# Performance work log

Measured on AMD Instinct MI355X. Metric: run time of the kernel, lower is better.

The kernel has to match this reference:

```python
import jax, jax.numpy as jnp
import numpy as np

N_NODES = 30000
N_REL = 200
N_EDGES = 150000
N_EDGES_NHOP = 30000
NFEAT = 100
NHID = 100
REL_DIM = 100
NHEADS = 2
ALPHA = 0.2  # leaky relu slope


def setup_inputs() -> dict:
    key = jax.random.key(0)
    ks = jax.random.split(key, 16)
    s = 0.1
    D = NHEADS * NHID
    inp = {}
    inp["entity_embeddings"] = jax.random.normal(ks[0], (N_NODES, NFEAT), jnp.float32)
    inp["relation_embed"] = jax.random.normal(ks[1], (N_REL, REL_DIM), jnp.float32)
    inp["edge_list"] = jax.random.randint(ks[2], (2, N_EDGES), 0, N_NODES)
    inp["edge_type"] = jax.random.randint(ks[3], (N_EDGES,), 0, N_REL)
    inp["edge_embed"] = jax.random.normal(ks[4], (N_EDGES, REL_DIM), jnp.float32)
    inp["edge_list_nhop"] = jax.random.randint(ks[5], (2, N_EDGES_NHOP), 0, N_NODES)
    inp["edge_type_nhop"] = jax.random.randint(ks[6], (N_EDGES_NHOP, 2), 0, N_REL)
    inp["entity_embeddings_mapping"] = jax.random.normal(ks[7], (N_NODES, NFEAT), jnp.float32)
    # learned params (xavier-like scale)
    inp["a_heads"] = jax.random.normal(ks[8], (NHEADS, NHID, 2 * NFEAT + REL_DIM), jnp.float32) * s
    inp["a2_heads"] = jax.random.normal(ks[9], (NHEADS, NHID), jnp.float32) * s
    inp["W"] = jax.random.normal(ks[10], (REL_DIM, D), jnp.float32) * s
    inp["a_out"] = jax.random.normal(ks[11], (D, 3 * D), jnp.float32) * s
    inp["a2_out"] = jax.random.normal(ks[12], (D,), jnp.float32) * s
    return inp


def _att_layer(x, src, dst, edge_embed, a, a2, n_nodes, concat):
    # Sparse graph attention (KBGAT style). a: [out, 2*in + rel_dim].
    in_dim = x.shape[1]
    a_src, a_dst, a_rel = a[:, :in_dim], a[:, in_dim:2 * in_dim], a[:, 2 * in_dim:]
    # edge_m = a @ cat(x[src], x[dst], edge_embed)^T, computed without the big concat
    edge_m = x[src] @ a_src.T + x[dst] @ a_dst.T + edge_embed @ a_rel.T  # [E, out]
    powers = -jax.nn.leaky_relu(edge_m @ a2, ALPHA)                      # [E]
    edge_e = jnp.exp(powers)                                             # [E]
    e_rowsum = jax.ops.segment_sum(edge_e, src, num_segments=n_nodes)    # [N]
    e_rowsum = jnp.where(e_rowsum == 0.0, 1e-12, e_rowsum)
    h = jax.ops.segment_sum(edge_e[:, None] * edge_m, src, num_segments=n_nodes)  # [N, out]
    h = h / e_rowsum[:, None]
    return jax.nn.elu(h) if concat else h


def reference(entity_embeddings, relation_embed, edge_list, edge_type, edge_embed,
              edge_list_nhop, edge_type_nhop, entity_embeddings_mapping,
              a_heads, a2_heads, W, a_out, a2_out):
    N = entity_embeddings.shape[0]
    src = jnp.concatenate([edge_list[0], edge_list_nhop[0]])
    dst = jnp.concatenate([edge_list[1], edge_list_nhop[1]])
    # 2-hop edge embedding = sum of the two relation embeddings on the path
    ee_nhop = relation_embed[edge_type_nhop[:, 0]] + relation_embed[edge_type_nhop[:, 1]]
    ee1 = jnp.concatenate([edge_embed, ee_nhop], axis=0)
    h1 = _att_layer(entity_embeddings, src, dst, ee1, a_heads[0], a2_heads[0], N, True)
    h2 = _att_layer(entity_embeddings, src, dst, ee1, a_heads[1], a2_heads[1], N, True)
    h = jnp.concatenate([h1, h2], axis=1)  # [N, 2*nhid]; dropout p=0 (eval)
    out_relation = relation_embed @ W      # [R, 2*nhid]
    ee2 = jnp.concatenate([out_relation[edge_type],
                           out_relation[edge_type_nhop[:, 0]] + out_relation[edge_type_nhop[:, 1]]],
                          axis=0)
    out_entity = _att_layer(h, src, dst, ee2, a_out, a2_out, N, False)
    return jax.nn.elu(out_entity), out_relation
```

## Files before the change

kernel.cpp:

```cpp
#include <hip/hip_runtime.h>

#define N_NODES 30000
#define E1 150000
#define EN 30000
#define ET 180000
#define LALPHA 0.2f
#define NB_SCAN 118

typedef unsigned int u32;
typedef unsigned short u16;
typedef __attribute__((ext_vector_type(8))) short short8;
typedef __attribute__((ext_vector_type(4))) short short4v;
typedef __attribute__((ext_vector_type(4))) float f32x4;

__device__ __forceinline__ float bf2f(u16 u){ return __uint_as_float(((u32)u)<<16); }
__device__ __forceinline__ float2 bfp2(u32 u){
  return make_float2(__uint_as_float(u<<16), __uint_as_float(u & 0xffff0000u));
}
__device__ __forceinline__ u16 f2bf(float f){
  u32 x = __float_as_uint(f);
  return (u16)((x + 0x7fffu + ((x>>16)&1u)) >> 16);
}
__device__ __forceinline__ u32 pk(float x, float y){
  return ((u32)f2bf(x)) | (((u32)f2bf(y))<<16);
}
__device__ __forceinline__ float wredf(float v){
  #pragma unroll
  for(int o=32;o>0;o>>=1) v += __shfl_xor(v, o, 64);
  return v;
}
__device__ __forceinline__ float eluf(float y){ return (y>0.f)? y : expm1f(y); }
__device__ __forceinline__ float ld1(const void* p, int i, int f){
  return f ? ((const float*)p)[i] : bf2f(((const u16*)p)[i]);
}
__device__ __forceinline__ float2 ldp(const void* p, int i, int f){
  if(f){ return ((const float2*)p)[i]; }
  return bfp2(((const u32*)p)[i]);
}
__device__ __forceinline__ void st1(void* p, int i, float v, int f){
  if(f) ((float*)p)[i] = v; else ((u16*)p)[i] = f2bf(v);
}

__device__ __forceinline__ short8 frag_zero(){
  short8 r;
  #pragma unroll
  for(int i=0;i<8;i++) r[i]=0;
  return r;
}
__device__ __forceinline__ short8 ldfragb(const u16* p, int idx){
  short8 r;
  short4v lo = *(const short4v*)(p+idx);
  short4v hi = *(const short4v*)(p+idx+4);
  #pragma unroll
  for(int i=0;i<4;i++){ r[i]=lo[i]; r[4+i]=hi[i]; }
  return r;
}
__device__ __forceinline__ short8 ldfragb_p4(const u16* p, int idx){
  short8 r=frag_zero();
  short4v lo = *(const short4v*)(p+idx);
  #pragma unroll
  for(int i=0;i<4;i++) r[i]=lo[i];
  return r;
}
__device__ __forceinline__ short8 ldfrag(const void* p, int idx, int f){
  short8 r;
  if(f){
    const float* fp=(const float*)p+idx;
    #pragma unroll
    for(int i=0;i<8;i++) r[i]=(short)f2bf(fp[i]);
  } else {
    return ldfragb((const u16*)p, idx);
  }
  return r;
}
__device__ __forceinline__ short8 ldfrag_p4(const void* p, int idx, int f){
  short8 r=frag_zero();
  if(f){
    const float* fp=(const float*)p+idx;
    #pragma unroll
    for(int i=0;i<4;i++) r[i]=(short)f2bf(fp[i]);
  } else {
    return ldfragb_p4((const u16*)p, idx);
  }
  return r;
}

__global__ void k_detect(const u32* x, int* flag){
  int t = threadIdx.x;
  int c = 0;
  #pragma unroll
  for(int i=0;i<4;i++){
    u32 v = x[t*4+i];
    u32 lo = v & 0xffffu;
    u32 e = (lo>>7)&0xffu;
    c += (lo==0u || (e>=100u && e<=140u)) ? 1 : 0;
  }
  __shared__ int sd[256];
  sd[t]=c; __syncthreads();
  for(int o=128;o>0;o>>=1){ if(t<o) sd[t]+=sd[t+o]; __syncthreads(); }
  if(t==0) *flag = (sd[0] > 512) ? 0 : 1;
}

__global__ void k_prep(const void* ent, const void* ah, const void* ao, const void* ee,
                       u16* entB, u16* ahB, u16* aoB, u16* eeB, int ws_ok, const int* flag){
  int f = *flag;
  int gid = blockIdx.x*256 + threadIdx.x;
  int stride = gridDim.x*256;
  const int T0=750000, T1=765000, T2=795000, T3=795000+3750000;
  int lim = (f && ws_ok) ? T3 : T2;
  for(int i=gid; i<lim; i+=stride){
    const void* src; u16* dst; int g;
    if(i<T0){ src=ent; dst=entB; g=i; }
    else if(i<T1){ src=ah; dst=ahB; g=i-T0; }
    else if(i<T2){ src=ao; dst=aoB; g=i-T1; }
    else { src=ee; dst=eeB; g=i-T2; }
    if(f){
      float4 v = ((const float4*)src)[g];
      short4v o;
      o[0]=(short)f2bf(v.x); o[1]=(short)f2bf(v.y);
      o[2]=(short)f2bf(v.z); o[3]=(short)f2bf(v.w);
      ((short4v*)dst)[g] = o;
    } else {
      ((short4v*)dst)[g] = ((const short4v*)src)[g];
    }
  }
}

__global__ void k_outrel(const void* rel, const void* W, float* outrel, void* out, const int* flag){
  int f = *flag;
  int t = blockIdx.x*blockDim.x + threadIdx.x;
  if(t >= 200*200) return;
  int r = t / 200, j = t - r*200;
  float acc = 0.f;
  for(int k=0;k<100;k++) acc += ld1(rel, r*100+k, f) * ld1(W, k*200+j, f);
  outrel[t] = acc;
  st1(out, 6000000 + t, acc, f);
}

__global__ void k_small_b(const void* ah, const void* a2h, const void* ao, const void* a2o,
                          float* b1, float* b2, const int* flag){
  int f = *flag;
  int i = blockIdx.x*4 + (threadIdx.x>>6);
  int L = threadIdx.x & 63;
  if(i >= 1200) return;
  float a = 0.f;
  if(i < 600){
    int hd = i/300, k = i - hd*300;
    for(int j=L; j<100; j+=64)
      a += ld1(a2h, hd*100+j, f) * ld1(ah, hd*30000 + j*300 + k, f);
    a = wredf(a);
    if(L==0) b1[i] = a;
  } else {
    int k = i - 600;
    for(int j=L; j<200; j+=64)
      a += ld1(a2o, j, f) * ld1(ao, j*600 + k, f);
    a = wredf(a);
    if(L==0) b2[k] = a;
  }
}

__global__ void k_small_c(const void* rel, const float* outrel, const float* b1, const float* b2,
                          float* c1, float* c2, const int* flag){
  int f = *flag;
  int i = blockIdx.x*4 + (threadIdx.x>>6);
  int L = threadIdx.x & 63;
  if(i >= 600) return;
  float a = 0.f;
  if(i < 400){
    int hd = i/200, r = i - hd*200;
    for(int k=L; k<100; k+=64)
      a += b1[hd*300+200+k] * ld1(rel, r*100+k, f);
    a = wredf(a);
    if(L==0) c1[i] = a;
  } else {
    int r = i - 400;
    for(int k=L; k<200; k+=64)
      a += b2[400+k] * outrel[r*200+k];
    a = wredf(a);
    if(L==0) c2[r] = a;
  }
}

__global__ void k_count(const int* src1, const int* srcN, int* cnt){
  int e = blockIdx.x*256 + threadIdx.x;
  if(e>=ET) return;
  int s = (e<E1)? src1[e] : srcN[e-E1];
  atomicAdd(&cnt[s],1);
}

__global__ void k_scan1(const int* cnt, int* ofs, int* bsum){
  __shared__ int sd[256];
  int b=blockIdx.x, t=threadIdx.x;
  int idx=b*256+t;
  int v=(idx<N_NODES)? cnt[idx] : 0;
  sd[t]=v; __syncthreads();
  for(int o=1;o<256;o<<=1){
    int u=(t>=o)? sd[t-o]:0;
    __syncthreads();
    sd[t]+=u; __syncthreads();
  }
  if(idx<N_NODES) ofs[idx]=sd[t]-v;
  if(t==255) bsum[b]=sd[255];
}

__global__ void k_scan2(const int* bsum, int* bstart, int* ofs){
  __shared__ int sd[128];
  int t=threadIdx.x;
  int v=(t<NB_SCAN)? bsum[t]:0;
  sd[t]=v; __syncthreads();
  for(int o=1;o<128;o<<=1){
    int u=(t>=o)? sd[t-o]:0;
    __syncthreads();
    sd[t]+=u; __syncthreads();
  }
  if(t<NB_SCAN) bstart[t]=sd[t]-v;
  if(t==127) ofs[N_NODES]=sd[127];
}

__global__ void k_scan3(int* ofs, int* cur, const int* bstart){
  int b=blockIdx.x, t=threadIdx.x;
  int idx=b*256+t;
  if(idx>=N_NODES) return;
  int v = ofs[idx] + bstart[b];
  ofs[idx]=v; cur[idx]=v;
}

__global__ void k_scatter(const int* src1, const int* srcN, int* cur, int* eord){
  int e = blockIdx.x*256 + threadIdx.x;
  if(e>=ET) return;
  int s = (e<E1)? src1[e] : srcN[e-E1];
  int p = atomicAdd(&cur[s],1);
  eord[p]=e;
}

__global__ void k_q1(const u32* entB2, const float* b1, float* q1){
  int n = blockIdx.x*4 + (threadIdx.x>>6);
  if(n>=N_NODES) return;
  int L = threadIdx.x & 63;
  float d00=0,d01=0,d10=0,d11=0;
  if(L<50){
    float2 xv = bfp2(entB2[n*50+L]);
    int k0=2*L;
    d00 = xv.x*b1[k0]     + xv.y*b1[k0+1];
    d01 = xv.x*b1[100+k0] + xv.y*b1[100+k0+1];
    d10 = xv.x*b1[300+k0] + xv.y*b1[300+k0+1];
    d11 = xv.x*b1[400+k0] + xv.y*b1[400+k0+1];
  }
  d00=wredf(d00); d01=wredf(d01); d10=wredf(d10); d11=wredf(d11);
  if(L==0){ q1[n*4+0]=d00; q1[n*4+1]=d01; q1[n*4+2]=d10; q1[n*4+3]=d11; }
}

__global__ __launch_bounds__(256) void k_edge1g(const void* ee, const u16* eeB, int ws_ok,
    const int* src1, const int* dst1, const float* b1, const float* q1,
    float* w1, const int* flag){
  int f = *flag;
  const void* eeP = (f && ws_ok) ? (const void*)eeB : ee;
  int fe = (f && ws_ok) ? 0 : f;
  int wid = threadIdx.x>>6, l = threadIdx.x&63;
  int lr = l&15, lg = l>>4;
  int m0 = blockIdx.x*128 + wid*32;
  short8 bfr[4];
  #pragma unroll
  for(int ks=0;ks<4;ks++){
    int kb = ks*32 + lg*8;
    short8 b = frag_zero();
    if(lr<2){
      const float* bp = b1 + (lr==0? 200:500);
      #pragma unroll
      for(int i=0;i<8;i++){ int k=kb+i; if(k<100) b[i]=(short)f2bf(bp[k]); }
    }
    bfr[ks]=b;
  }
  int row0 = m0 + lr, row1 = m0 + 16 + lr;
  bool ok0 = row0 < E1, ok1 = row1 < E1;
  f32x4 acc0=(f32x4){0,0,0,0}, acc1=(f32x4){0,0,0,0};
  #pragma unroll
  for(int ks=0;ks<4;ks++){
    int kb = ks*32 + lg*8;
    short8 a0 = frag_zero(), a1 = frag_zero();
    if(ok0){
      if(kb+8<=100) a0 = ldfrag(eeP, row0*100+kb, fe);
      else if(kb<100) a0 = ldfrag_p4(eeP, row0*100+kb, fe);
    }
    if(ok1){
      if(kb+8<=100) a1 = ldfrag(eeP, row1*100+kb, fe);
      else if(kb<100) a1 = ldfrag_p4(eeP, row1*100+kb, fe);
    }
    acc0 = __builtin_amdgcn_mfma_f32_16x16x32_bf16(a0, bfr[ks], acc0, 0,0,0);
    acc1 = __builtin_amdgcn_mfma_f32_16x16x32_bf16(a1, bfr[ks], acc1, 0,0,0);
  }
  if(lr<2){
    #pragma unroll
    for(int mi=0;mi<2;mi++){
      #pragma unroll
      for(int r=0;r<4;r++){
        int e = m0 + mi*16 + lg*4 + r;
        if(e<E1){
          float rv = (mi==0)? acc0[r] : acc1[r];
          int s=src1[e], d=dst1[e];
          float p = q1[s*4+lr*2] + q1[d*4+lr*2+1] + rv;
          p = (p>=0.f)? p : LALPHA*p;
          w1[2*e + lr] = expf(-p);
        }
      }
    }
  }
}

__global__ void k_edge1b(const int* etn, const int* srcN, const int* dstN,
                         const float* c1, const float* q1, float* w1){
  int en = blockIdx.x*256+threadIdx.x;
  if(en>=EN) return;
  int t0=etn[en*2], t1=etn[en*2+1];
  float r0 = c1[t0]+c1[t1];
  float r1 = c1[200+t0]+c1[200+t1];
  int s=srcN[en], d=dstN[en];
  float p0 = q1[s*4+0]+q1[d*4+1]+r0;
  float p1 = q1[s*4+2]+q1[d*4+3]+r1;
  p0=(p0>=0.f)?p0:LALPHA*p0;
  p1=(p1>=0.f)?p1:LALPHA*p1;
  w1[2*(E1+en)]   = expf(-p0);
  w1[2*(E1+en)+1] = expf(-p1);
}

__global__ void k_acc1(const int* ofs, const int* eord,
                       const int* dst1, const int* dstN, const int* etn,
                       const u32* entB2, const void* ee, const u32* eeB32, int ws_ok,
                       const void* rel,
                       const float2* w1p, u32* Gq, float* rs1, const int* flag){
  int f = *flag;
  int use_pack = (f==1) && ws_ok;
  int n = blockIdx.x*4 + (threadIdx.x>>6);
  if(n>=N_NODES) return;
  int L = threadIdx.x & 63;
  int beg = ofs[n], end = ofs[n+1];
  float av0x=0,av0y=0,av1x=0,av1y=0, aw0x=0,aw0y=0,aw1x=0,aw1y=0;
  float r0=0, r1=0;
  int i = beg;
  for(; i+3<end; i+=4){
    int e[4]; float2 w[4]; int d[4];
    #pragma unroll
    for(int u=0;u<4;u++) e[u]=eord[i+u];
    #pragma unroll
    for(int u=0;u<4;u++){ w[u]=w1p[e[u]]; d[u]=(e[u]<E1)? dst1[e[u]] : dstN[e[u]-E1]; }
    r0 += w[0].x+w[1].x+w[2].x+w[3].x;
    r1 += w[0].y+w[1].y+w[2].y+w[3].y;
    if(L<50){
      float2 xv[4], vv[4];
      #pragma unroll
      for(int u=0;u<4;u++) xv[u]=bfp2(entB2[d[u]*50+L]);
      #pragma unroll
      for(int u=0;u<4;u++){
        if(e[u]<E1){ vv[u] = use_pack? bfp2(eeB32[e[u]*50+L]) : ldp(ee, e[u]*50+L, f); }
        else { int en=e[u]-E1; int t0=etn[en*2], t1=etn[en*2+1];
               float2 a=ldp(rel,t0*50+L,f), b=ldp(rel,t1*50+L,f);
               vv[u]=make_float2(a.x+b.x, a.y+b.y); }
      }
      #pragma unroll
      for(int u=0;u<4;u++){
        av0x += w[u].x*xv[u].x; av0y += w[u].x*xv[u].y;
        av1x += w[u].y*xv[u].x; av1y += w[u].y*xv[u].y;
        aw0x += w[u].x*vv[u].x; aw0y += w[u].x*vv[u].y;
        aw1x += w[u].y*vv[u].x; aw1y += w[u].y*vv[u].y;
      }
    }
  }
  for(; i<end; ++i){
    int e0 = eord[i];
    float2 wa = w1p[e0];
    r0 += wa.x; r1 += wa.y;
    int d0 = (e0<E1)? dst1[e0] : dstN[e0-E1];
    if(L<50){
      float2 x0 = bfp2(entB2[d0*50+L]);
      float2 v0;
      if(e0<E1){ v0 = use_pack? bfp2(eeB32[e0*50+L]) : ldp(ee, e0*50+L, f); }
      else { int en=e0-E1; int t0=etn[en*2], t1=etn[en*2+1];
             float2 a=ldp(rel,t0*50+L,f), b=ldp(rel,t1*50+L,f);
             v0=make_float2(a.x+b.x, a.y+b.y); }
      av0x += wa.x*x0.x; av0y += wa.x*x0.y;
      av1x += wa.y*x0.x; av1y += wa.y*x0.y;
      aw0x += wa.x*v0.x; aw0y += wa.x*v0.y;
      aw1x += wa.y*v0.x; aw1y += wa.y*v0.y;
    }
  }
  float i0 = (r0==0.f)? 0.f : 1.f/r0;
  float i1 = (r1==0.f)? 0.f : 1.f/r1;
  if(L<50){
    u32* g0 = Gq + n*100;
    u32* g1 = Gq + 3000000 + n*100;
    g0[L]    = pk(av0x*i0, av0y*i0);
    g0[50+L] = pk(aw0x*i0, aw0y*i0);
    g1[L]    = pk(av1x*i1, av1y*i1);
    g1[50+L] = pk(aw1x*i1, aw1y*i1);
  }
  if(L==0){ rs1[n]=r0; rs1[N_NODES+n]=r1; }
}

__global__ __launch_bounds__(256) void k_gemm1m(const u16* G, const u16* ahB, const u16* entB,
                        const float* rs1, u16* h){
  int hd = blockIdx.y;
  int wid = threadIdx.x>>6, l = threadIdx.x&63;
  int lr = l&15, lg = l>>4;
  int m0 = blockIdx.x*32;
  int row0 = m0 + lr, row1 = m0 + 16 + lr;
  bool hi_ok = (m0+16) < N_NODES;
  const u16* Gh0 = G + hd*6000000 + row0*200;
  const u16* Gh1 = G + hd*6000000 + row1*200;
  const u16* A = ahB + hd*30000;
  f32x4 acc[2][2];
  #pragma unroll
  for(int mi=0;mi<2;mi++)
    #pragma unroll
    for(int ntl=0;ntl<2;ntl++) acc[mi][ntl]=(f32x4){0.f,0.f,0.f,0.f};
  #pragma unroll
  for(int k0=0;k0<100;k0+=32){
    int kb = k0 + lg*8;
    short8 a0 = (kb+8<=100)? ldfragb(entB, row0*100+kb)
              : (kb<100    ? ldfragb_p4(entB, row0*100+kb) : frag_zero());
    short8 a1 = frag_zero();
    if(hi_ok){
      if(kb+8<=100) a1 = ldfragb(entB, row1*100+kb);
      else if(kb<100) a1 = ldfragb_p4(entB, row1*100+kb);
    }
    #pragma unroll
    for(int ntl=0;ntl<2;ntl++){
      int j = (ntl*4+wid)*16 + lr;
      short8 b = frag_zero();
      if(j<100){
        if(kb+8<=100) b = ldfragb(A, j*300 + kb);
        else if(kb<100) b = ldfragb_p4(A, j*300 + kb);
      }
      acc[0][ntl] = __builtin_amdgcn_mfma_f32_16x16x32_bf16(a0, b, acc[0][ntl], 0,0,0);
      acc[1][ntl] = __builtin_amdgcn_mfma_f32_16x16x32_bf16(a1, b, acc[1][ntl], 0,0,0);
    }
  }
  #pragma unroll
  for(int k0=0;k0<200;k0+=32){
    int kb = k0 + lg*8;
    short8 a0 = (kb+8<=200)? ldfragb(Gh0, kb) : frag_zero();
    short8 a1 = (hi_ok && kb+8<=200)? ldfragb(Gh1, kb) : frag_zero();
    #pragma unroll
    for(int ntl=0;ntl<2;ntl++){
      int j = (ntl*4+wid)*16 + lr;
      short8 b = (j<100 && kb+8<=200)? ldfragb(A, j*300 + 100 + kb) : frag_zero();
      acc[0][ntl] = __builtin_amdgcn_mfma_f32_16x16x32_bf16(a0, b, acc[0][ntl], 0,0,0);
      acc[1][ntl] = __builtin_amdgcn_mfma_f32_16x16x32_bf16(a1, b, acc[1][ntl], 0,0,0);
    }
  }
  #pragma unroll
  for(int mi=0;mi<2;mi++){
    if(mi==1 && !hi_ok) break;
    #pragma unroll
    for(int r=0;r<4;r++){
      int rr = m0 + mi*16 + lg*4 + r;
      float sc = (rs1[hd*N_NODES+rr]==0.f)? 0.f : 1.f;
      #pragma unroll
      for(int ntl=0;ntl<2;ntl++){
        int j = (ntl*4+wid)*16 + lr;
        if(j<100) h[rr*200 + hd*100 + j] = f2bf(eluf(acc[mi][ntl][r]*sc));
      }
    }
  }
}

__global__ void k_q2(const u32* h32, const float* b2, float* q2){
  int n = blockIdx.x*4 + (threadIdx.x>>6);
  if(n>=N_NODES) return;
  int L = threadIdx.x&63;
  float ds=0, dd=0;
  if(L<50){
    float2 a = bfp2(h32[n*100+2*L]);
    float2 b = bfp2(h32[n*100+2*L+1]);
    int k0=4*L;
    ds = a.x*b2[k0]+a.y*b2[k0+1]+b.x*b2[k0+2]+b.y*b2[k0+3];
    dd = a.x*b2[200+k0]+a.y*b2[200+k0+1]+b.x*b2[200+k0+2]+b.y*b2[200+k0+3];
  }
  ds=wredf(ds); dd=wredf(dd);
  if(L==0){ q2[n*2]=ds; q2[n*2+1]=dd; }
}

__global__ void k_edge2(const int* src1,const int* dst1,const int* srcN,const int* dstN,
                        const int* et, const int* etn, const float* c2, const float* q2, float* w2){
  int e = blockIdx.x*256+threadIdx.x;
  if(e>=ET) return;
  int s,d; float r;
  if(e<E1){ s=src1[e]; d=dst1[e]; r = c2[et[e]]; }
  else { int en=e-E1; s=srcN[en]; d=dstN[en]; r = c2[etn[en*2]]+c2[etn[en*2+1]]; }
  float p = q2[s*2] + q2[d*2+1] + r;
  p = (p>=0.f)? p : LALPHA*p;
  w2[e] = expf(-p);
}

__global__ void k_acc2(const int* ofs, const int* eord,
                       const int* dst1,const int* dstN, const int* et,const int* etn,
                       const u32* h32, const float4* or4, const float* w2,
                       u32* Gq, float* rs2){
  const uint2* h2 = (const uint2*)h32;
  int n = blockIdx.x*4 + (threadIdx.x>>6);
  if(n>=N_NODES) return;
  int L = threadIdx.x&63;
  int beg=ofs[n], end=ofs[n+1];
  float rv=0;
  float avx=0,avy=0,avz=0,avw=0, awx=0,awy=0,awz=0,aww=0;
  int i=beg;
  for(; i+3<end; i+=4){
    int e[4]; float wv[4]; int d[4];
    #pragma unroll
    for(int u=0;u<4;u++) e[u]=eord[i+u];
    #pragma unroll
    for(int u=0;u<4;u++){ wv[u]=w2[e[u]]; d[u]=(e[u]<E1)? dst1[e[u]]:dstN[e[u]-E1]; }
    rv += wv[0]+wv[1]+wv[2]+wv[3];
    if(L<50){
      float2 ha[4], hb[4]; float4 o[4];
      #pragma unroll
      for(int u=0;u<4;u++){ uint2 hv = h2[d[u]*50+L]; ha[u]=bfp2(hv.x); hb[u]=bfp2(hv.y); }
      #pragma unroll
      for(int u=0;u<4;u++){
        if(e[u]<E1){ o[u] = or4[et[e[u]]*50+L]; }
        else { int en=e[u]-E1; float4 a=or4[etn[en*2]*50+L], b=or4[etn[en*2+1]*50+L];
               o[u]=make_float4(a.x+b.x,a.y+b.y,a.z+b.z,a.w+b.w); }
      }
      #pragma unroll
      for(int u=0;u<4;u++){
        avx += wv[u]*ha[u].x; avy += wv[u]*ha[u].y;
        avz += wv[u]*hb[u].x; avw += wv[u]*hb[u].y;
        awx += wv[u]*o[u].x;  awy += wv[u]*o[u].y;
        awz += wv[u]*o[u].z;  aww += wv[u]*o[u].w;
      }
    }
  }
  for(; i<end; ++i){
    int e0=eord[i];
    float w0=w2[e0];
    rv += w0;
    int d0 = (e0<E1)? dst1[e0]:dstN[e0-E1];
    if(L<50){
      uint2 hv = h2[d0*50+L];
      float2 ha0=bfp2(hv.x), hb0=bfp2(hv.y);
      float4 o0;
      if(e0<E1){ o0 = or4[et[e0]*50+L]; }
      else { int en=e0-E1; float4 a=or4[etn[en*2]*50+L], b=or4[etn[en*2+1]*50+L];
             o0=make_float4(a.x+b.x,a.y+b.y,a.z+b.z,a.w+b.w); }
      avx += w0*ha0.x; avy += w0*ha0.y; avz += w0*hb0.x; avw += w0*hb0.y;
      awx += w0*o0.x; awy += w0*o0.y; awz += w0*o0.z; aww += w0*o0.w;
    }
  }
  float inv = (rv==0.f)? 0.f : 1.f/rv;
  if(L<50){
    u32* g = Gq + n*200;
    g[2*L]       = pk(avx*inv, avy*inv);
    g[2*L+1]     = pk(avz*inv, avw*inv);
    g[100+2*L]   = pk(awx*inv, awy*inv);
    g[100+2*L+1] = pk(awz*inv, aww*inv);
  }
  if(L==0) rs2[n]=rv;
}

__global__ __launch_bounds__(256) void k_gemm2m(const u16* G, const u16* aoB, const u16* h,
                        const float* rs2, void* out, const int* flag){
  int f = *flag;
  int wid = threadIdx.x>>6, l = threadIdx.x&63;
  int lr = l&15, lg = l>>4;
  int m0 = blockIdx.x*32;
  int row0 = m0 + lr, row1 = m0 + 16 + lr;
  bool hi_ok = (m0+16) < N_NODES;
  const u16* h0 = h + row0*200;
  const u16* h1 = h + row1*200;
  const u16* g0 = G + row0*400;
  const u16* g1 = G + row1*400;
  f32x4 acc[2][4];
  #pragma unroll
  for(int mi=0;mi<2;mi++)
    #pragma unroll
    for(int ntl=0;ntl<4;ntl++) acc[mi][ntl]=(f32x4){0.f,0.f,0.f,0.f};
  #pragma unroll
  for(int k0=0;k0<200;k0+=32){
    int kb = k0 + lg*8;
    short8 a0 = (kb+8<=200)? ldfragb(h0, kb) : frag_zero();
    short8 a1 = (hi_ok && kb+8<=200)? ldfragb(h1, kb) : frag_zero();
    #pragma unroll
    for(int ntl=0;ntl<4;ntl++){
      int j = (ntl*4+wid)*16 + lr;
      short8 b = (j<200 && kb+8<=200)? ldfragb(aoB, j*600 + kb) : frag_zero();
      acc[0][ntl] = __builtin_amdgcn_mfma_f32_16x16x32_bf16(a0, b, acc[0][ntl], 0,0,0);
      acc[1][ntl] = __builtin_amdgcn_mfma_f32_16x16x32_bf16(a1, b, acc[1][ntl], 0,0,0);
    }
  }
  #pragma unroll
  for(int k0=0;k0<400;k0+=32){
    int kb = k0 + lg*8;
    short8 a0 = (kb+8<=400)? ldfragb(g0, kb) : frag_zero();
    short8 a1 = (hi_ok && kb+8<=400)? ldfragb(g1, kb) : frag_zero();
    #pragma unroll
    for(int ntl=0;ntl<4;ntl++){
      int j = (ntl*4+wid)*16 + lr;
      short8 b = (j<200 && kb+8<=400)? ldfragb(aoB, j*600 + 200 + kb) : frag_zero();
      acc[0][ntl] = __builtin_amdgcn_mfma_f32_16x16x32_bf16(a0, b, acc[0][ntl], 0,0,0);
      acc[1][ntl] = __builtin_amdgcn_mfma_f32_16x16x32_bf16(a1, b, acc[1][ntl], 0,0,0);
    }
  }
  #pragma unroll
  for(int mi=0;mi<2;mi++){
    if(mi==1 && !hi_ok) break;
    #pragma unroll
    for(int r=0;r<4;r++){
      int rr = m0 + mi*16 + lg*4 + r;
      float sc = (rs2[rr]==0.f)? 0.f : 1.f;
      #pragma unroll
      for(int ntl=0;ntl<4;ntl++){
        int j = (ntl*4+wid)*16 + lr;
        if(j<200) st1(out, rr*200 + j, eluf(acc[mi][ntl][r]*sc), f);
      }
    }
  }
}

extern "C" void kernel_launch(void* const* d_in, const int* in_sizes, int n_in,
                              void* d_out, int out_size, void* d_ws, size_t ws_size,
                              hipStream_t stream) {
  const void* ent = d_in[0];
  const void* rel = d_in[1];
  const int* el  = (const int*)d_in[2];
  const int* et  = (const int*)d_in[3];
  const void* ee  = d_in[4];
  const int* eln = (const int*)d_in[5];
  const int* etn = (const int*)d_in[6];
  const void* ah  = d_in[8];
  const void* a2h = d_in[9];
  const void* W   = d_in[10];
  const void* ao  = d_in[11];
  const void* a2o = d_in[12];

  float* wsf    = (float*)d_ws;
  int*   flag   = (int*)wsf;
  float* outrel = wsf+4;
  float* b1     = wsf+40008;
  float* b2     = wsf+40608;
  float* c1     = wsf+41208;
  float* c2     = wsf+41608;
  float* q1     = wsf+41808;
  float* q2     = wsf+161808;
  float* w1     = wsf+221808;
  float* w2     = wsf+581808;
  float* rs1    = wsf+761808;
  float* rs2    = wsf+821808;
  int*   ofs    = (int*)(wsf+851808);
  int*   cnt    = ofs+30001;
  int*   cur    = cnt+30000;
  int*   eord   = cur+30000;
  int*   bsum   = (int*)(wsf+1121812);
  int*   bstart = bsum+128;
  u16*   G      = (u16*)(wsf+1122072);
  u16*   h      = (u16*)(wsf+7122072);
  u16*   entB   = (u16*)(wsf+10122072);
  u16*   ahB    = (u16*)(wsf+11622072);
  u16*   aoB    = (u16*)(wsf+11652072);
  u16*   eeB    = (u16*)(wsf+11712072);
  int ws_ok = (ws_size >= (size_t)19212072*4) ? 1 : 0;

  const int* src1 = el;
  const int* dst1 = el + E1;
  const int* srcN = eln;
  const int* dstN = eln + EN;

  k_detect<<<1,256,0,stream>>>((const u32*)ent, flag);
  hipMemsetAsync(cnt, 0, 30000*sizeof(int), stream);
  k_prep<<<2048,256,0,stream>>>(ent, ah, ao, ee, entB, ahB, aoB, eeB, ws_ok, flag);
  k_small_b<<<300,256,0,stream>>>(ah,a2h,ao,a2o,b1,b2,flag);
  k_outrel<<<(200*200+255)/256,256,0,stream>>>(rel, W, outrel, d_out, flag);
  k_small_c<<<150,256,0,stream>>>(rel, outrel, b1, b2, c1, c2, flag);
  k_count<<<(ET+255)/256,256,0,stream>>>(src1, srcN, cnt);
  k_scan1<<<NB_SCAN,256,0,stream>>>(cnt, ofs, bsum);
  k_scan2<<<1,128,0,stream>>>(bsum, bstart, ofs);
  k_scan3<<<NB_SCAN,256,0,stream>>>(ofs, cur, bstart);
  k_scatter<<<(ET+255)/256,256,0,stream>>>(src1, srcN, cur, eord);
  k_q1<<<(N_NODES+3)/4,256,0,stream>>>((const u32*)entB, b1, q1);
  k_edge1g<<<(E1+127)/128,256,0,stream>>>(ee, eeB, ws_ok, src1, dst1, b1, q1, w1, flag);
  k_edge1b<<<(EN+255)/256,256,0,stream>>>(etn, srcN, dstN, c1, q1, w1);
  k_acc1<<<(N_NODES+3)/4,256,0,stream>>>(ofs, eord, dst1, dstN, etn,
                                         (const u32*)entB, ee, (const u32*)eeB, ws_ok,
                                         rel, (const float2*)w1, (u32*)G, rs1, flag);
  dim3 g1grid((N_NODES+31)/32, 2);
  k_gemm1m<<<g1grid,256,0,stream>>>(G, ahB, entB, rs1, h);
  k_q2<<<(N_NODES+3)/4,256,0,stream>>>((const u32*)h, b2, q2);
  k_edge2<<<(ET+255)/256,256,0,stream>>>(src1, dst1, srcN, dstN, et, etn, c2, q2, w2);
  k_acc2<<<(N_NODES+3)/4,256,0,stream>>>(ofs, eord, dst1, dstN, et, etn,
                                         (const u32*)h, (const float4*)outrel, w2, (u32*)G, rs2);
  k_gemm2m<<<(N_NODES+31)/32,256,0,stream>>>(G, aoB, h, rs2, d_out, flag);
}
```

Baseline: 257.4 us.

## Interleave h and aggregated features into one row buffer for the second GEMM

```diff
diff --git a/kernel.cpp b/kernel.cpp
--- a/kernel.cpp
+++ b/kernel.cpp
@@ -54,6 +54,9 @@
   #pragma unroll
   for(int i=0;i<4;i++){ r[i]=lo[i]; r[4+i]=hi[i]; }
   return r;
+}
+__device__ __forceinline__ short8 ldfragb16(const u16* p, int idx){
+  return *(const short8*)(p+idx);
 }
 __device__ __forceinline__ short8 ldfragb_p4(const u16* p, int idx){
   short8 r=frag_zero();
@@ -397,7 +400,7 @@
 }
 
 __global__ __launch_bounds__(256) void k_gemm1m(const u16* G, const u16* ahB, const u16* entB,
-                        const float* rs1, u16* h){
+                        const float* rs1, u16* Gx2){
   int hd = blockIdx.y;
   int wid = threadIdx.x>>6, l = threadIdx.x&63;
   int lr = l&15, lg = l>>4;
@@ -457,20 +460,21 @@
       #pragma unroll
       for(int ntl=0;ntl<2;ntl++){
         int j = (ntl*4+wid)*16 + lr;
-        if(j<100) h[rr*200 + hd*100 + j] = f2bf(eluf(acc[mi][ntl][r]*sc));
-      }
-    }
-  }
-}
-
-__global__ void k_q2(const u32* h32, const float* b2, float* q2){
+        if(j<100) Gx2[rr*600 + hd*100 + j] = f2bf(eluf(acc[mi][ntl][r]*sc));
+      }
+    }
+  }
+}
+
+__global__ void k_q2(const uint2* hq, const float* b2, float* q2){
   int n = blockIdx.x*4 + (threadIdx.x>>6);
   if(n>=N_NODES) return;
   int L = threadIdx.x&63;
   float ds=0, dd=0;
   if(L<50){
-    float2 a = bfp2(h32[n*100+2*L]);
-    float2 b = bfp2(h32[n*100+2*L+1]);
+    uint2 hv = hq[n*150+L];
+    float2 a = bfp2(hv.x);
+    float2 b = bfp2(hv.y);
     int k0=4*L;
     ds = a.x*b2[k0]+a.y*b2[k0+1]+b.x*b2[k0+2]+b.y*b2[k0+3];
     dd = a.x*b2[200+k0]+a.y*b2[200+k0+1]+b.x*b2[200+k0+2]+b.y*b2[200+k0+3];
@@ -493,9 +497,9 @@
 
 __global__ void k_acc2(const int* ofs, const int* eord,
                        const int* dst1,const int* dstN, const int* et,const int* etn,
-                       const u32* h32, const float4* or4, const float* w2,
-                       u32* Gq, float* rs2){
-  const uint2* h2 = (const uint2*)h32;
+                       u32* Gx2u, const float4* or4, const float* w2,
+                       float* rs2){
+  const uint2* h2 = (const uint2*)Gx2u;
   int n = blockIdx.x*4 + (threadIdx.x>>6);
   if(n>=N_NODES) return;
   int L = threadIdx.x&63;
@@ -513,7 +517,7 @@
     if(L<50){
       float2 ha[4], hb[4]; float4 o[4];
       #pragma unroll
-      for(int u=0;u<4;u++){ uint2 hv = h2[d[u]*50+L]; ha[u]=bfp2(hv.x); hb[u]=bfp2(hv.y); }
+      for(int u=0;u<4;u++){ uint2 hv = h2[d[u]*150+L]; ha[u]=bfp2(hv.x); hb[u]=bfp2(hv.y); }
       #pragma unroll
       for(int u=0;u<4;u++){
         if(e[u]<E1){ o[u] = or4[et[e[u]]*50+L]; }
@@ -535,7 +539,7 @@
     rv += w0;
     int d0 = (e0<E1)? dst1[e0]:dstN[e0-E1];
     if(L<50){
-      uint2 hv = h2[d0*50+L];
+      uint2 hv = h2[d0*150+L];
       float2 ha0=bfp2(hv.x), hb0=bfp2(hv.y);
       float4 o0;
       if(e0<E1){ o0 = or4[et[e0]*50+L]; }
@@ -547,7 +551,7 @@
   }
   float inv = (rv==0.f)? 0.f : 1.f/rv;
   if(L<50){
-    u32* g = Gq + n*200;
+    u32* g = Gx2u + n*300 + 100;
     g[2*L]       = pk(avx*inv, avy*inv);
     g[2*L+1]     = pk(avz*inv, avw*inv);
     g[100+2*L]   = pk(awx*inv, awy*inv);
@@ -556,7 +560,7 @@
   if(L==0) rs2[n]=rv;
 }
 
-__global__ __launch_bounds__(256) void k_gemm2m(const u16* G, const u16* aoB, const u16* h,
+__global__ __launch_bounds__(256) void k_gemm2m(const u16* Gx2, const u16* aoB,
                         const float* rs2, void* out, const int* flag){
   int f = *flag;
   int wid = threadIdx.x>>6, l = threadIdx.x&63;
@@ -564,37 +568,23 @@
   int m0 = blockIdx.x*32;
   int row0 = m0 + lr, row1 = m0 + 16 + lr;
   bool hi_ok = (m0+16) < N_NODES;
-  const u16* h0 = h + row0*200;
-  const u16* h1 = h + row1*200;
-  const u16* g0 = G + row0*400;
-  const u16* g1 = G + row1*400;
+  const u16* a0p = Gx2 + row0*600;
+  const u16* a1p = Gx2 + row1*600;
   f32x4 acc[2][4];
   #pragma unroll
   for(int mi=0;mi<2;mi++)
     #pragma unroll
     for(int ntl=0;ntl<4;ntl++) acc[mi][ntl]=(f32x4){0.f,0.f,0.f,0.f};
   #pragma unroll
-  for(int k0=0;k0<200;k0+=32){
+  for(int k0=0;k0<600;k0+=32){
     int kb = k0 + lg*8;
-    short8 a0 = (kb+8<=200)? ldfragb(h0, kb) : frag_zero();
-    short8 a1 = (hi_ok && kb+8<=200)? ldfragb(h1, kb) : frag_zero();
+    bool kok = (kb+8<=600);
+    short8 a0 = kok? ldfragb16(a0p, kb) : frag_zero();
+    short8 a1 = (hi_ok && kok)? ldfragb16(a1p, kb) : frag_zero();
     #pragma unroll
     for(int ntl=0;ntl<4;ntl++){
       int j = (ntl*4+wid)*16 + lr;
-      short8 b = (j<200 && kb+8<=200)? ldfragb(aoB, j*600 + kb) : frag_zero();
-      acc[0][ntl] = __builtin_amdgcn_mfma_f32_16x16x32_bf16(a0, b, acc[0][ntl], 0,0,0);
-      acc[1][ntl] = __builtin_amdgcn_mfma_f32_16x16x32_bf16(a1, b, acc[1][ntl], 0,0,0);
-    }
-  }
-  #pragma unroll
-  for(int k0=0;k0<400;k0+=32){
-    int kb = k0 + lg*8;
-    short8 a0 = (kb+8<=400)? ldfragb(g0, kb) : frag_zero();
-    short8 a1 = (hi_ok && kb+8<=400)? ldfragb(g1, kb) : frag_zero();
-    #pragma unroll
-    for(int ntl=0;ntl<4;ntl++){
-      int j = (ntl*4+wid)*16 + lr;
-      short8 b = (j<200 && kb+8<=400)? ldfragb(aoB, j*600 + 200 + kb) : frag_zero();
+      short8 b = (j<200 && kok)? ldfragb16(aoB, j*600 + kb) : frag_zero();
       acc[0][ntl] = __builtin_amdgcn_mfma_f32_16x16x32_bf16(a0, b, acc[0][ntl], 0,0,0);
       acc[1][ntl] = __builtin_amdgcn_mfma_f32_16x16x32_bf16(a1, b, acc[1][ntl], 0,0,0);
     }
@@ -651,11 +641,11 @@
   int*   bsum   = (int*)(wsf+1121812);
   int*   bstart = bsum+128;
   u16*   G      = (u16*)(wsf+1122072);
-  u16*   h      = (u16*)(wsf+7122072);
   u16*   entB   = (u16*)(wsf+10122072);
   u16*   ahB    = (u16*)(wsf+11622072);
   u16*   aoB    = (u16*)(wsf+11652072);
   u16*   eeB    = (u16*)(wsf+11712072);
+  u16*   Gx2    = (u16*)(wsf+11712072);
   int ws_ok = (ws_size >= (size_t)19212072*4) ? 1 : 0;
 
   const int* src1 = el;
@@ -681,10 +671,10 @@
                                          (const u32*)entB, ee, (const u32*)eeB, ws_ok,
                                          rel, (const float2*)w1, (u32*)G, rs1, flag);
   dim3 g1grid((N_NODES+31)/32, 2);
-  k_gemm1m<<<g1grid,256,0,stream>>>(G, ahB, entB, rs1, h);
-  k_q2<<<(N_NODES+3)/4,256,0,stream>>>((const u32*)h, b2, q2);
+  k_gemm1m<<<g1grid,256,0,stream>>>(G, ahB, entB, rs1, Gx2);
+  k_q2<<<(N_NODES+3)/4,256,0,stream>>>((const uint2*)Gx2, b2, q2);
   k_edge2<<<(ET+255)/256,256,0,stream>>>(src1, dst1, srcN, dstN, et, etn, c2, q2, w2);
   k_acc2<<<(N_NODES+3)/4,256,0,stream>>>(ofs, eord, dst1, dstN, et, etn,
-                                         (const u32*)h, (const float4*)outrel, w2, (u32*)G, rs2);
-  k_gemm2m<<<(N_NODES+31)/32,256,0,stream>>>(G, aoB, h, rs2, d_out, flag);
-}
+                                         (u32*)Gx2, (const float4*)outrel, w2, rs2);
+  k_gemm2m<<<(N_NODES+31)/32,256,0,stream>>>(Gx2, aoB, rs2, d_out, flag);
+}
```

Result: no change. 257.5 us (+0.0%).
